# Performance work log

Hardware: AMD Instinct MI355X
Metric: run time of the kernel (lower is better)

The kernel has to match this reference:

```python
import jax, jax.numpy as jnp
import numpy as np


def deform_conv2d(x, w, offset, mask, pad):
    """Modulated deformable conv (DCNv2), stride 1, dilation 1, groups 1.
    x: [B,C,H,W], w: [Co,C,kh,kw], offset: [B,2*K,H,W] (y,x per tap), mask: [B,K,H,W].
    Output spatial size equals input (pad = (k-1)//2).
    """
    B, C, H, W = x.shape
    Co, _, kh, kw = w.shape
    K = kh * kw
    off = offset.reshape(B, K, 2, H, W)
    dy, dx = off[:, :, 0], off[:, :, 1]               # [B,K,H,W]
    ky, kx = jnp.meshgrid(jnp.arange(kh), jnp.arange(kw), indexing='ij')
    ky = ky.reshape(K).astype(x.dtype)
    kx = kx.reshape(K).astype(x.dtype)
    hh = jnp.arange(H, dtype=x.dtype)
    ww = jnp.arange(W, dtype=x.dtype)
    # sampling coords: p0 + p_k + delta p_k
    py = hh[None, None, :, None] - pad + ky[None, :, None, None] + dy  # [B,K,H,W]
    px = ww[None, None, None, :] - pad + kx[None, :, None, None] + dx
    y0 = jnp.floor(py)
    x0 = jnp.floor(px)
    wy = py - y0
    wx = px - x0
    y0i = y0.astype(jnp.int32)
    x0i = x0.astype(jnp.int32)
    x_flat = x.reshape(B, C, H * W)

    def gather(yi, xi):
        valid = (yi >= 0) & (yi < H) & (xi >= 0) & (xi < W)  # zero padding outside
        idx = jnp.clip(yi, 0, H - 1) * W + jnp.clip(xi, 0, W - 1)
        g = jnp.take_along_axis(x_flat, idx.reshape(B, 1, K * H * W), axis=2)
        g = g.reshape(B, C, K, H, W)
        return g * valid[:, None].astype(x.dtype)

    v00 = gather(y0i, x0i)
    v01 = gather(y0i, x0i + 1)
    v10 = gather(y0i + 1, x0i)
    v11 = gather(y0i + 1, x0i + 1)
    wy_ = wy[:, None]  # [B,1,K,H,W]
    wx_ = wx[:, None]
    samp = (v00 * (1 - wy_) * (1 - wx_) + v01 * (1 - wy_) * wx_
            + v10 * wy_ * (1 - wx_) + v11 * wy_ * wx_)   # [B,C,K,H,W]
    # masked weighted accumulation == conv over sampled taps
    return jnp.einsum('bckhw,bkhw,ock->bohw', samp, mask, w.reshape(Co, C, K))


def setup_inputs() -> dict:
    key = jax.random.key(0)
    ks = jax.random.split(key, 10)
    B, C, H, W, Co = 4, 64, 64, 64, 64
    inp = {
        'x': jax.random.normal(ks[0], (B, C, H, W), dtype=jnp.float32),
        'filter1': jax.random.normal(ks[1], (Co, C, 3, 3), dtype=jnp.float32) * 0.05,
        'offset1': jax.random.normal(ks[2], (B, 2 * 9, H, W), dtype=jnp.float32),
        'mask1': jax.random.uniform(ks[3], (B, 9, H, W), dtype=jnp.float32),
        'filter2': jax.random.normal(ks[4], (Co, C, 5, 5), dtype=jnp.float32) * 0.03,
        'offset2': jax.random.normal(ks[5], (B, 2 * 25, H, W), dtype=jnp.float32),
        'mask2': jax.random.uniform(ks[6], (B, 25, H, W), dtype=jnp.float32),
        'filter3': jax.random.normal(ks[7], (Co, C, 7, 7), dtype=jnp.float32) * 0.02,
        'offset3': jax.random.normal(ks[8], (B, 2 * 49, H, W), dtype=jnp.float32),
        'mask3': jax.random.uniform(ks[9], (B, 49, H, W), dtype=jnp.float32),
    }
    return inp


def reference(x, filter1, offset1, mask1, filter2, offset2, mask2, filter3, offset3, mask3):
    part1 = deform_conv2d(x, filter1, offset1, mask1, pad=1)  # 3x3
    part2 = deform_conv2d(x, filter2, offset2, mask2, pad=2)  # 5x5
    part3 = deform_conv2d(x, filter3, offset3, mask3, pad=3)  # 7x7
    return jnp.concatenate((part1, part2, part3), axis=1)
```

## Files before the change

kernel.cpp:

```cpp
#include <hip/hip_runtime.h>
#include <hip/hip_bf16.h>


typedef __attribute__((ext_vector_type(8))) short bf16x8;
typedef __attribute__((ext_vector_type(8))) unsigned short u16x8;
typedef __attribute__((ext_vector_type(4))) float f32x4;

#define WR 16
#define WC 30
#define WS 68
#define SLS 20

__device__ __forceinline__ float b2f(unsigned short u) {
    return __uint_as_float(((unsigned)u) << 16);
}
__device__ __forceinline__ unsigned short f2bf(float f) {
    __hip_bfloat16 h = __float2bfloat16(f);
    return *reinterpret_cast<unsigned short*>(&h);
}

__global__ __launch_bounds__(256) void k_prep(
    const float* __restrict__ x,
    const float* __restrict__ f1, const float* __restrict__ f2, const float* __restrict__ f3,
    unsigned short* __restrict__ xTb,
    unsigned short* __restrict__ wp1, unsigned short* __restrict__ wp2, unsigned short* __restrict__ wp3) {
    __shared__ float tile[64][65];
    int bid = blockIdx.x;
    int tid = threadIdx.x;
    if (bid < 256) {
        int b = bid >> 6, h = bid & 63;
        {
            int w = tid & 63, c4 = tid >> 6;
            const float* xp = x + (((b * 64) * 64 + h) * 64) + w;
            #pragma unroll
            for (int i = 0; i < 16; ++i) {
                int c = c4 * 16 + i;
                tile[c][w] = xp[c * 4096];
            }
        }
        __syncthreads();
        {
            int c = tid & 63, w4 = tid >> 6;
            unsigned short* op = xTb + (((b * 64 + h) * 64) * 64) + c;
            #pragma unroll
            for (int i = 0; i < 16; ++i) {
                int ww = w4 * 16 + i;
                op[ww * 64] = f2bf(tile[c][ww]);
            }
        }
    } else {
        int idx = (bid - 256) * 256 + tid;
        const float* f; unsigned short* wp; int K, rel;
        if (idx < 36864)       { f = f1; wp = wp1; K = 9;  rel = idx; }
        else if (idx < 139264) { f = f2; wp = wp2; K = 25; rel = idx - 36864; }
        else                   { f = f3; wp = wp3; K = 49; rel = idx - 139264; }
        int c = rel & 63;
        int o = (rel >> 6) & 63;
        int k = rel >> 12;
        wp[rel] = f2bf(f[(o * 64 + c) * K + k]);
    }
}

template<int KW, int PAD, int KS, int KE>
__device__ __forceinline__ void run_range(
    const float* __restrict__ offp, const float* __restrict__ mskp,
    const unsigned short* __restrict__ wp, const unsigned short* __restrict__ win,
    const unsigned short* __restrict__ xb,
    int h, int pw, int ylo, int cxlo, int ch0, int l16, f32x4 acc[4]) {

    #pragma unroll 2
    for (int k = KS; k < KE; ++k) {
        int ky = k / KW, kx = k - ky * KW;
        float dy = offp[k * 8192];
        float dx = offp[k * 8192 + 4096];
        float mk = mskp[k * 4096];
        float py = (float)(h - PAD + ky) + dy;
        float px = (float)(pw - PAD + kx) + dx;
        float y0f = floorf(py), x0f = floorf(px);
        float wy = py - y0f, wx = px - x0f;
        int y0 = (int)y0f, x0 = (int)x0f;
        int y1 = y0 + 1, x1 = x0 + 1;
        float fy0 = ((unsigned)y0 < 64u) ? (1.f - wy) * mk : 0.f;
        float fy1 = ((unsigned)y1 < 64u) ? wy * mk         : 0.f;
        float gx0 = ((unsigned)x0 < 64u) ? (1.f - wx)      : 0.f;
        float gx1 = ((unsigned)x1 < 64u) ? wx              : 0.f;
        float w00 = fy0 * gx0, w01 = fy0 * gx1, w10 = fy1 * gx0, w11 = fy1 * gx1;

        int r0 = y0 - ylo, r1 = r0 + 1;
        int c0 = x0 - cxlo, c1 = c0 + 1;
        bool oow = ((w00 != 0.f) & (((unsigned)r0 >= WR) | ((unsigned)c0 >= WC)))
                 | ((w01 != 0.f) & (((unsigned)r0 >= WR) | ((unsigned)c1 >= WC)))
                 | ((w10 != 0.f) & (((unsigned)r1 >= WR) | ((unsigned)c0 >= WC)))
                 | ((w11 != 0.f) & (((unsigned)r1 >= WR) | ((unsigned)c1 >= WC)));
        int r0c = min(max(r0, 0), WR - 1), r1c = min(max(r1, 0), WR - 1);
        int c0c = min(max(c0, 0), WC - 1), c1c = min(max(c1, 0), WC - 1);
        int p00 = (r0c * WC + c0c) * WS;
        int p01 = (r0c * WC + c1c) * WS;
        int p10 = (r1c * WC + c0c) * WS;
        int p11 = (r1c * WC + c1c) * WS;

        u16x8 g00a = *(const u16x8*)(win + p00 + ch0);
        u16x8 g01a = *(const u16x8*)(win + p01 + ch0);
        u16x8 g10a = *(const u16x8*)(win + p10 + ch0);
        u16x8 g11a = *(const u16x8*)(win + p11 + ch0);
        u16x8 g00b = *(const u16x8*)(win + p00 + 32 + ch0);
        u16x8 g01b = *(const u16x8*)(win + p01 + 32 + ch0);
        u16x8 g10b = *(const u16x8*)(win + p10 + 32 + ch0);
        u16x8 g11b = *(const u16x8*)(win + p11 + 32 + ch0);

        if (oow) {
            int y0g = min(max(y0, 0), 63), y1g = min(max(y1, 0), 63);
            int x0g = min(max(x0, 0), 63), x1g = min(max(x1, 0), 63);
            int o00 = ((y0g << 6) + x0g) << 6;
            int o01 = ((y0g << 6) + x1g) << 6;
            int o10 = ((y1g << 6) + x0g) << 6;
            int o11 = ((y1g << 6) + x1g) << 6;
            g00a = *(const u16x8*)(xb + o00 + ch0);
            g01a = *(const u16x8*)(xb + o01 + ch0);
            g10a = *(const u16x8*)(xb + o10 + ch0);
            g11a = *(const u16x8*)(xb + o11 + ch0);
            g00b = *(const u16x8*)(xb + o00 + 32 + ch0);
            g01b = *(const u16x8*)(xb + o01 + 32 + ch0);
            g10b = *(const u16x8*)(xb + o10 + 32 + ch0);
            g11b = *(const u16x8*)(xb + o11 + 32 + ch0);
        }

        union { bf16x8 v; unsigned short u[8]; } A0, A1;
        #pragma unroll
        for (int j = 0; j < 8; ++j) {
            float s0 = w00 * b2f(g00a[j]) + w01 * b2f(g01a[j])
                     + w10 * b2f(g10a[j]) + w11 * b2f(g11a[j]);
            float s1 = w00 * b2f(g00b[j]) + w01 * b2f(g01b[j])
                     + w10 * b2f(g10b[j]) + w11 * b2f(g11b[j]);
            A0.u[j] = f2bf(s0);
            A1.u[j] = f2bf(s1);
        }

        const unsigned short* wpk = wp + (k << 12);
        #pragma unroll
        for (int ct = 0; ct < 4; ++ct) {
            const unsigned short* wr = wpk + ((ct * 16 + l16) << 6);
            bf16x8 b0 = *(const bf16x8*)(wr + ch0);
            bf16x8 b1 = *(const bf16x8*)(wr + 32 + ch0);
            acc[ct] = __builtin_amdgcn_mfma_f32_16x16x32_bf16(A0.v, b0, acc[ct], 0, 0, 0);
            acc[ct] = __builtin_amdgcn_mfma_f32_16x16x32_bf16(A1.v, b1, acc[ct], 0, 0, 0);
        }
    }
}

__global__ __launch_bounds__(256) void k_dcn(
    const unsigned short* __restrict__ xTb,
    const float* __restrict__ off1, const float* __restrict__ msk1, const unsigned short* __restrict__ wp1,
    const float* __restrict__ off2, const float* __restrict__ msk2, const unsigned short* __restrict__ wp2,
    const float* __restrict__ off3, const float* __restrict__ msk3, const unsigned short* __restrict__ wp3,
    float* __restrict__ out) {

    __shared__ __align__(16) unsigned char smem[WR * WC * WS * 2];
    unsigned short* win = (unsigned short*)smem;
    float* slab = (float*)smem;

    int tile = blockIdx.x;
    int b  = tile >> 8;
    int h  = (tile >> 2) & 63;
    int w0 = (tile & 3) << 4;

    int tid  = threadIdx.x;
    int wv   = tid >> 6;
    int lane = tid & 63;
    int quad = lane >> 4;
    int l16  = lane & 15;
    int ylo  = h - 7, cxlo = w0 - 7;

    const unsigned short* xb = xTb + ((size_t)b << 18);

    {
        int j = tid & 7;
        for (int p = tid >> 3; p < WR * WC; p += 32) {
            int r = p / WC, cc = p - r * WC;
            int y = min(max(ylo + r, 0), 63);
            int x = min(max(cxlo + cc, 0), 63);
            *(u16x8*)(win + p * WS + j * 8) =
                *(const u16x8*)(xb + (((y << 6) + x) << 6) + j * 8);
        }
    }
    __syncthreads();

    int pw  = w0 + l16;
    int ch0 = quad << 3;
    const float* o1p = off1 + (b * 18) * 4096 + (h << 6) + pw;
    const float* m1p = msk1 + (b * 9)  * 4096 + (h << 6) + pw;
    const float* o2p = off2 + (b * 50) * 4096 + (h << 6) + pw;
    const float* m2p = msk2 + (b * 25) * 4096 + (h << 6) + pw;
    const float* o3p = off3 + (b * 98) * 4096 + (h << 6) + pw;
    const float* m3p = msk3 + (b * 49) * 4096 + (h << 6) + pw;

    f32x4 accA[4], accB[4];
    #pragma unroll
    for (int i = 0; i < 4; ++i) { accA[i] = (f32x4){0,0,0,0}; accB[i] = (f32x4){0,0,0,0}; }
    int slabA, slabB = -1;

    if (wv == 0) {
        run_range<3,1,0,9>  (o1p, m1p, wp1, win, xb, h, pw, ylo, cxlo, ch0, l16, accA);
        run_range<5,2,0,12> (o2p, m2p, wp2, win, xb, h, pw, ylo, cxlo, ch0, l16, accB);
        slabA = 0; slabB = 1;
    } else if (wv == 1) {
        run_range<5,2,12,25>(o2p, m2p, wp2, win, xb, h, pw, ylo, cxlo, ch0, l16, accA);
        run_range<7,3,0,8>  (o3p, m3p, wp3, win, xb, h, pw, ylo, cxlo, ch0, l16, accB);
        slabA = 2; slabB = 3;
    } else if (wv == 2) {
        run_range<7,3,8,29> (o3p, m3p, wp3, win, xb, h, pw, ylo, cxlo, ch0, l16, accA);
        slabA = 4;
    } else {
        run_range<7,3,29,49>(o3p, m3p, wp3, win, xb, h, pw, ylo, cxlo, ch0, l16, accA);
        slabA = 5;
    }

    __syncthreads();

    #pragma unroll
    for (int ct = 0; ct < 4; ++ct) {
        *(f32x4*)&slab[slabA * 1280 + (ct * 16 + l16) * SLS + quad * 4] = accA[ct];
    }
    if (slabB >= 0) {
        #pragma unroll
        for (int ct = 0; ct < 4; ++ct) {
            *(f32x4*)&slab[slabB * 1280 + (ct * 16 + l16) * SLS + quad * 4] = accB[ct];
        }
    }
    __syncthreads();

    for (int it = tid; it < 768; it += 256) {
        int g = it & 3;
        int o = it >> 2;
        int oo = o & 63;
        int base = oo * SLS + g * 4;
        f32x4 v;
        if (o < 64) {
            v = *(const f32x4*)&slab[base];
        } else if (o < 128) {
            f32x4 a0 = *(const f32x4*)&slab[1280 + base];
            f32x4 a1 = *(const f32x4*)&slab[2560 + base];
            #pragma unroll
            for (int r = 0; r < 4; ++r) v[r] = a0[r] + a1[r];
        } else {
            f32x4 a0 = *(const f32x4*)&slab[3840 + base];
            f32x4 a1 = *(const f32x4*)&slab[5120 + base];
            f32x4 a2 = *(const f32x4*)&slab[6400 + base];
            #pragma unroll
            for (int r = 0; r < 4; ++r) v[r] = a0[r] + (a1[r] + a2[r]);
        }
        *(f32x4*)&out[(((size_t)b * 192 + o) * 64 + h) * 64 + w0 + g * 4] = v;
    }
}

extern "C" void kernel_launch(void* const* d_in, const int* in_sizes, int n_in,
                              void* d_out, int out_size, void* d_ws, size_t ws_size,
                              hipStream_t stream) {
    const float* x    = (const float*)d_in[0];
    const float* f1   = (const float*)d_in[1];
    const float* off1 = (const float*)d_in[2];
    const float* msk1 = (const float*)d_in[3];
    const float* f2   = (const float*)d_in[4];
    const float* off2 = (const float*)d_in[5];
    const float* msk2 = (const float*)d_in[6];
    const float* f3   = (const float*)d_in[7];
    const float* off3 = (const float*)d_in[8];
    const float* msk3 = (const float*)d_in[9];
    float* out = (float*)d_out;

    unsigned short* xTb = (unsigned short*)d_ws;
    unsigned short* wp1 = xTb + 4 * 64 * 64 * 64;
    unsigned short* wp2 = wp1 + 9 * 4096;
    unsigned short* wp3 = wp2 + 25 * 4096;

    k_prep<<<dim3(1584), dim3(256), 0, stream>>>(x, f1, f2, f3, xTb, wp1, wp2, wp3);
    k_dcn<<<dim3(1024), dim3(256), 0, stream>>>(xTb,
                                                off1, msk1, wp1,
                                                off2, msk2, wp2,
                                                off3, msk3, wp3,
                                                out);
}
```

Before: 195.6 us.

## Split deformable taps across eight waves and pack bilinear math into float2

```diff
diff --git a/kernel.cpp b/kernel.cpp
--- a/kernel.cpp
+++ b/kernel.cpp
@@ -5,18 +5,22 @@
 typedef __attribute__((ext_vector_type(8))) short bf16x8;
 typedef __attribute__((ext_vector_type(8))) unsigned short u16x8;
 typedef __attribute__((ext_vector_type(4))) float f32x4;
+typedef __attribute__((ext_vector_type(2))) float f32x2;
 
 #define WR 16
 #define WC 30
 #define WS 68
 #define SLS 20
 
-__device__ __forceinline__ float b2f(unsigned short u) {
-    return __uint_as_float(((unsigned)u) << 16);
-}
 __device__ __forceinline__ unsigned short f2bf(float f) {
     __hip_bfloat16 h = __float2bfloat16(f);
     return *reinterpret_cast<unsigned short*>(&h);
+}
+__device__ __forceinline__ f32x2 unpk(unsigned u) {
+    f32x2 r;
+    r[0] = __uint_as_float(u << 16);
+    r[1] = __uint_as_float(u & 0xffff0000u);
+    return r;
 }
 
 __global__ __launch_bounds__(256) void k_prep(
@@ -99,14 +103,16 @@
         int p10 = (r1c * WC + c0c) * WS;
         int p11 = (r1c * WC + c1c) * WS;
 
-        u16x8 g00a = *(const u16x8*)(win + p00 + ch0);
-        u16x8 g01a = *(const u16x8*)(win + p01 + ch0);
-        u16x8 g10a = *(const u16x8*)(win + p10 + ch0);
-        u16x8 g11a = *(const u16x8*)(win + p11 + ch0);
-        u16x8 g00b = *(const u16x8*)(win + p00 + 32 + ch0);
-        u16x8 g01b = *(const u16x8*)(win + p01 + 32 + ch0);
-        u16x8 g10b = *(const u16x8*)(win + p10 + 32 + ch0);
-        u16x8 g11b = *(const u16x8*)(win + p11 + 32 + ch0);
+        union U { u16x8 v; unsigned u[4]; };
+        U g00a, g01a, g10a, g11a, g00b, g01b, g10b, g11b;
+        g00a.v = *(const u16x8*)(win + p00 + ch0);
+        g01a.v = *(const u16x8*)(win + p01 + ch0);
+        g10a.v = *(const u16x8*)(win + p10 + ch0);
+        g11a.v = *(const u16x8*)(win + p11 + ch0);
+        g00b.v = *(const u16x8*)(win + p00 + 32 + ch0);
+        g01b.v = *(const u16x8*)(win + p01 + 32 + ch0);
+        g10b.v = *(const u16x8*)(win + p10 + 32 + ch0);
+        g11b.v = *(const u16x8*)(win + p11 + 32 + ch0);
 
         if (oow) {
             int y0g = min(max(y0, 0), 63), y1g = min(max(y1, 0), 63);
@@ -115,25 +121,28 @@
             int o01 = ((y0g << 6) + x1g) << 6;
             int o10 = ((y1g << 6) + x0g) << 6;
             int o11 = ((y1g << 6) + x1g) << 6;
-            g00a = *(const u16x8*)(xb + o00 + ch0);
-            g01a = *(const u16x8*)(xb + o01 + ch0);
-            g10a = *(const u16x8*)(xb + o10 + ch0);
-            g11a = *(const u16x8*)(xb + o11 + ch0);
-            g00b = *(const u16x8*)(xb + o00 + 32 + ch0);
-            g01b = *(const u16x8*)(xb + o01 + 32 + ch0);
-            g10b = *(const u16x8*)(xb + o10 + 32 + ch0);
-            g11b = *(const u16x8*)(xb + o11 + 32 + ch0);
-        }
-
+            g00a.v = *(const u16x8*)(xb + o00 + ch0);
+            g01a.v = *(const u16x8*)(xb + o01 + ch0);
+            g10a.v = *(const u16x8*)(xb + o10 + ch0);
+            g11a.v = *(const u16x8*)(xb + o11 + ch0);
+            g00b.v = *(const u16x8*)(xb + o00 + 32 + ch0);
+            g01b.v = *(const u16x8*)(xb + o01 + 32 + ch0);
+            g10b.v = *(const u16x8*)(xb + o10 + 32 + ch0);
+            g11b.v = *(const u16x8*)(xb + o11 + 32 + ch0);
+        }
+
+        f32x2 W00 = {w00, w00}, W01 = {w01, w01}, W10 = {w10, w10}, W11 = {w11, w11};
         union { bf16x8 v; unsigned short u[8]; } A0, A1;
         #pragma unroll
-        for (int j = 0; j < 8; ++j) {
-            float s0 = w00 * b2f(g00a[j]) + w01 * b2f(g01a[j])
-                     + w10 * b2f(g10a[j]) + w11 * b2f(g11a[j]);
-            float s1 = w00 * b2f(g00b[j]) + w01 * b2f(g01b[j])
-                     + w10 * b2f(g10b[j]) + w11 * b2f(g11b[j]);
-            A0.u[j] = f2bf(s0);
-            A1.u[j] = f2bf(s1);
+        for (int j2 = 0; j2 < 4; ++j2) {
+            f32x2 s0 = W00 * unpk(g00a.u[j2]) + W01 * unpk(g01a.u[j2])
+                     + W10 * unpk(g10a.u[j2]) + W11 * unpk(g11a.u[j2]);
+            f32x2 s1 = W00 * unpk(g00b.u[j2]) + W01 * unpk(g01b.u[j2])
+                     + W10 * unpk(g10b.u[j2]) + W11 * unpk(g11b.u[j2]);
+            A0.u[2 * j2]     = f2bf(s0[0]);
+            A0.u[2 * j2 + 1] = f2bf(s0[1]);
+            A1.u[2 * j2]     = f2bf(s1[0]);
+            A1.u[2 * j2 + 1] = f2bf(s1[1]);
         }
 
         const unsigned short* wpk = wp + (k << 12);
@@ -148,7 +157,7 @@
     }
 }
 
-__global__ __launch_bounds__(256) void k_dcn(
+__global__ __launch_bounds__(512, 4) void k_dcn(
     const unsigned short* __restrict__ xTb,
     const float* __restrict__ off1, const float* __restrict__ msk1, const unsigned short* __restrict__ wp1,
     const float* __restrict__ off2, const float* __restrict__ msk2, const unsigned short* __restrict__ wp2,
@@ -175,7 +184,7 @@
 
     {
         int j = tid & 7;
-        for (int p = tid >> 3; p < WR * WC; p += 32) {
+        for (int p = tid >> 3; p < WR * WC; p += 64) {
             int r = p / WC, cc = p - r * WC;
             int y = min(max(ylo + r, 0), 63);
             int x = min(max(cxlo + cc, 0), 63);
@@ -199,20 +208,33 @@
     for (int i = 0; i < 4; ++i) { accA[i] = (f32x4){0,0,0,0}; accB[i] = (f32x4){0,0,0,0}; }
     int slabA, slabB = -1;
 
-    if (wv == 0) {
-        run_range<3,1,0,9>  (o1p, m1p, wp1, win, xb, h, pw, ylo, cxlo, ch0, l16, accA);
-        run_range<5,2,0,12> (o2p, m2p, wp2, win, xb, h, pw, ylo, cxlo, ch0, l16, accB);
-        slabA = 0; slabB = 1;
-    } else if (wv == 1) {
-        run_range<5,2,12,25>(o2p, m2p, wp2, win, xb, h, pw, ylo, cxlo, ch0, l16, accA);
-        run_range<7,3,0,8>  (o3p, m3p, wp3, win, xb, h, pw, ylo, cxlo, ch0, l16, accB);
-        slabA = 2; slabB = 3;
-    } else if (wv == 2) {
-        run_range<7,3,8,29> (o3p, m3p, wp3, win, xb, h, pw, ylo, cxlo, ch0, l16, accA);
-        slabA = 4;
-    } else {
-        run_range<7,3,29,49>(o3p, m3p, wp3, win, xb, h, pw, ylo, cxlo, ch0, l16, accA);
-        slabA = 5;
+    switch (wv) {
+        case 0:
+            run_range<3,1,0,9>  (o1p, m1p, wp1, win, xb, h, pw, ylo, cxlo, ch0, l16, accA);
+            slabA = 0; break;
+        case 1:
+            run_range<5,2,0,11> (o2p, m2p, wp2, win, xb, h, pw, ylo, cxlo, ch0, l16, accA);
+            slabA = 1; break;
+        case 2:
+            run_range<5,2,11,22>(o2p, m2p, wp2, win, xb, h, pw, ylo, cxlo, ch0, l16, accA);
+            slabA = 2; break;
+        case 3:
+            run_range<5,2,22,25>(o2p, m2p, wp2, win, xb, h, pw, ylo, cxlo, ch0, l16, accA);
+            slabA = 3;
+            run_range<7,3,0,8>  (o3p, m3p, wp3, win, xb, h, pw, ylo, cxlo, ch0, l16, accB);
+            slabB = 4; break;
+        case 4:
+            run_range<7,3,8,18> (o3p, m3p, wp3, win, xb, h, pw, ylo, cxlo, ch0, l16, accA);
+            slabA = 5; break;
+        case 5:
+            run_range<7,3,18,28>(o3p, m3p, wp3, win, xb, h, pw, ylo, cxlo, ch0, l16, accA);
+            slabA = 6; break;
+        case 6:
+            run_range<7,3,28,38>(o3p, m3p, wp3, win, xb, h, pw, ylo, cxlo, ch0, l16, accA);
+            slabA = 7; break;
+        default:
+            run_range<7,3,38,49>(o3p, m3p, wp3, win, xb, h, pw, ylo, cxlo, ch0, l16, accA);
+            slabA = 8; break;
     }
 
     __syncthreads();
@@ -229,7 +251,7 @@
     }
     __syncthreads();
 
-    for (int it = tid; it < 768; it += 256) {
+    for (int it = tid; it < 768; it += 512) {
         int g = it & 3;
         int o = it >> 2;
         int oo = o & 63;
@@ -238,16 +260,19 @@
         if (o < 64) {
             v = *(const f32x4*)&slab[base];
         } else if (o < 128) {
-            f32x4 a0 = *(const f32x4*)&slab[1280 + base];
-            f32x4 a1 = *(const f32x4*)&slab[2560 + base];
-            #pragma unroll
-            for (int r = 0; r < 4; ++r) v[r] = a0[r] + a1[r];
-        } else {
-            f32x4 a0 = *(const f32x4*)&slab[3840 + base];
-            f32x4 a1 = *(const f32x4*)&slab[5120 + base];
-            f32x4 a2 = *(const f32x4*)&slab[6400 + base];
+            f32x4 a0 = *(const f32x4*)&slab[1 * 1280 + base];
+            f32x4 a1 = *(const f32x4*)&slab[2 * 1280 + base];
+            f32x4 a2 = *(const f32x4*)&slab[3 * 1280 + base];
             #pragma unroll
             for (int r = 0; r < 4; ++r) v[r] = a0[r] + (a1[r] + a2[r]);
+        } else {
+            f32x4 a0 = *(const f32x4*)&slab[4 * 1280 + base];
+            f32x4 a1 = *(const f32x4*)&slab[5 * 1280 + base];
+            f32x4 a2 = *(const f32x4*)&slab[6 * 1280 + base];
+            f32x4 a3 = *(const f32x4*)&slab[7 * 1280 + base];
+            f32x4 a4 = *(const f32x4*)&slab[8 * 1280 + base];
+            #pragma unroll
+            for (int r = 0; r < 4; ++r) v[r] = (a0[r] + a1[r]) + (a2[r] + a3[r]) + a4[r];
         }
         *(f32x4*)&out[(((size_t)b * 192 + o) * 64 + h) * 64 + w0 + g * 4] = v;
     }
@@ -274,7 +299,7 @@
     unsigned short* wp3 = wp2 + 25 * 4096;
 
     k_prep<<<dim3(1584), dim3(256), 0, stream>>>(x, f1, f2, f3, xTb, wp1, wp2, wp3);
-    k_dcn<<<dim3(1024), dim3(256), 0, stream>>>(xTb,
+    k_dcn<<<dim3(1024), dim3(512), 0, stream>>>(xTb,
                                                 off1, msk1, wp1,
                                                 off2, msk2, wp2,
                                                 off3, msk3, wp3,
```

Measured after the change: 180.3 us. -7.9%, faster.

## Split channel halves and tap ranges across 16 waves per block

Applied to the files above, without the earlier changes.

```diff
diff --git a/kernel.cpp b/kernel.cpp
--- a/kernel.cpp
+++ b/kernel.cpp
@@ -5,18 +5,22 @@
 typedef __attribute__((ext_vector_type(8))) short bf16x8;
 typedef __attribute__((ext_vector_type(8))) unsigned short u16x8;
 typedef __attribute__((ext_vector_type(4))) float f32x4;
+typedef __attribute__((ext_vector_type(2))) float f32x2;
 
 #define WR 16
 #define WC 30
 #define WS 68
 #define SLS 20
 
-__device__ __forceinline__ float b2f(unsigned short u) {
-    return __uint_as_float(((unsigned)u) << 16);
-}
 __device__ __forceinline__ unsigned short f2bf(float f) {
     __hip_bfloat16 h = __float2bfloat16(f);
     return *reinterpret_cast<unsigned short*>(&h);
+}
+__device__ __forceinline__ f32x2 unpk(unsigned u) {
+    f32x2 r;
+    r[0] = __uint_as_float(u << 16);
+    r[1] = __uint_as_float(u & 0xffff0000u);
+    return r;
 }
 
 __global__ __launch_bounds__(256) void k_prep(
@@ -68,9 +72,9 @@
     const unsigned short* __restrict__ xb,
     int h, int pw, int ylo, int cxlo, int ch0, int l16, f32x4 acc[4]) {
 
-    #pragma unroll 2
+    #pragma unroll
     for (int k = KS; k < KE; ++k) {
-        int ky = k / KW, kx = k - ky * KW;
+        const int ky = k / KW, kx = k - ky * KW;
         float dy = offp[k * 8192];
         float dx = offp[k * 8192 + 4096];
         float mk = mskp[k * 4096];
@@ -94,61 +98,42 @@
                  | ((w11 != 0.f) & (((unsigned)r1 >= WR) | ((unsigned)c1 >= WC)));
         int r0c = min(max(r0, 0), WR - 1), r1c = min(max(r1, 0), WR - 1);
         int c0c = min(max(c0, 0), WC - 1), c1c = min(max(c1, 0), WC - 1);
-        int p00 = (r0c * WC + c0c) * WS;
-        int p01 = (r0c * WC + c1c) * WS;
-        int p10 = (r1c * WC + c0c) * WS;
-        int p11 = (r1c * WC + c1c) * WS;
-
-        u16x8 g00a = *(const u16x8*)(win + p00 + ch0);
-        u16x8 g01a = *(const u16x8*)(win + p01 + ch0);
-        u16x8 g10a = *(const u16x8*)(win + p10 + ch0);
-        u16x8 g11a = *(const u16x8*)(win + p11 + ch0);
-        u16x8 g00b = *(const u16x8*)(win + p00 + 32 + ch0);
-        u16x8 g01b = *(const u16x8*)(win + p01 + 32 + ch0);
-        u16x8 g10b = *(const u16x8*)(win + p10 + 32 + ch0);
-        u16x8 g11b = *(const u16x8*)(win + p11 + 32 + ch0);
+
+        union GU { u16x8 v; unsigned u[4]; } g00, g01, g10, g11;
+        g00.v = *(const u16x8*)(win + (r0c * WC + c0c) * WS + ch0);
+        g01.v = *(const u16x8*)(win + (r0c * WC + c1c) * WS + ch0);
+        g10.v = *(const u16x8*)(win + (r1c * WC + c0c) * WS + ch0);
+        g11.v = *(const u16x8*)(win + (r1c * WC + c1c) * WS + ch0);
 
         if (oow) {
             int y0g = min(max(y0, 0), 63), y1g = min(max(y1, 0), 63);
             int x0g = min(max(x0, 0), 63), x1g = min(max(x1, 0), 63);
-            int o00 = ((y0g << 6) + x0g) << 6;
-            int o01 = ((y0g << 6) + x1g) << 6;
-            int o10 = ((y1g << 6) + x0g) << 6;
-            int o11 = ((y1g << 6) + x1g) << 6;
-            g00a = *(const u16x8*)(xb + o00 + ch0);
-            g01a = *(const u16x8*)(xb + o01 + ch0);
-            g10a = *(const u16x8*)(xb + o10 + ch0);
-            g11a = *(const u16x8*)(xb + o11 + ch0);
-            g00b = *(const u16x8*)(xb + o00 + 32 + ch0);
-            g01b = *(const u16x8*)(xb + o01 + 32 + ch0);
-            g10b = *(const u16x8*)(xb + o10 + 32 + ch0);
-            g11b = *(const u16x8*)(xb + o11 + 32 + ch0);
-        }
-
-        union { bf16x8 v; unsigned short u[8]; } A0, A1;
-        #pragma unroll
-        for (int j = 0; j < 8; ++j) {
-            float s0 = w00 * b2f(g00a[j]) + w01 * b2f(g01a[j])
-                     + w10 * b2f(g10a[j]) + w11 * b2f(g11a[j]);
-            float s1 = w00 * b2f(g00b[j]) + w01 * b2f(g01b[j])
-                     + w10 * b2f(g10b[j]) + w11 * b2f(g11b[j]);
-            A0.u[j] = f2bf(s0);
-            A1.u[j] = f2bf(s1);
+            g00.v = *(const u16x8*)(xb + (((y0g << 6) + x0g) << 6) + ch0);
+            g01.v = *(const u16x8*)(xb + (((y0g << 6) + x1g) << 6) + ch0);
+            g10.v = *(const u16x8*)(xb + (((y1g << 6) + x0g) << 6) + ch0);
+            g11.v = *(const u16x8*)(xb + (((y1g << 6) + x1g) << 6) + ch0);
+        }
+
+        f32x2 W00 = {w00, w00}, W01 = {w01, w01}, W10 = {w10, w10}, W11 = {w11, w11};
+        union { bf16x8 v; unsigned short u[8]; } A;
+        #pragma unroll
+        for (int j = 0; j < 4; ++j) {
+            f32x2 s = W00 * unpk(g00.u[j]) + W01 * unpk(g01.u[j])
+                    + W10 * unpk(g10.u[j]) + W11 * unpk(g11.u[j]);
+            A.u[2 * j]     = f2bf(s[0]);
+            A.u[2 * j + 1] = f2bf(s[1]);
         }
 
         const unsigned short* wpk = wp + (k << 12);
         #pragma unroll
         for (int ct = 0; ct < 4; ++ct) {
-            const unsigned short* wr = wpk + ((ct * 16 + l16) << 6);
-            bf16x8 b0 = *(const bf16x8*)(wr + ch0);
-            bf16x8 b1 = *(const bf16x8*)(wr + 32 + ch0);
-            acc[ct] = __builtin_amdgcn_mfma_f32_16x16x32_bf16(A0.v, b0, acc[ct], 0, 0, 0);
-            acc[ct] = __builtin_amdgcn_mfma_f32_16x16x32_bf16(A1.v, b1, acc[ct], 0, 0, 0);
-        }
-    }
-}
-
-__global__ __launch_bounds__(256) void k_dcn(
+            bf16x8 bfr = *(const bf16x8*)(wpk + ((ct * 16 + l16) << 6) + ch0);
+            acc[ct] = __builtin_amdgcn_mfma_f32_16x16x32_bf16(A.v, bfr, acc[ct], 0, 0, 0);
+        }
+    }
+}
+
+__global__ __launch_bounds__(1024, 8) void k_dcn(
     const unsigned short* __restrict__ xTb,
     const float* __restrict__ off1, const float* __restrict__ msk1, const unsigned short* __restrict__ wp1,
     const float* __restrict__ off2, const float* __restrict__ msk2, const unsigned short* __restrict__ wp2,
@@ -164,18 +149,20 @@
     int h  = (tile >> 2) & 63;
     int w0 = (tile & 3) << 4;
 
-    int tid  = threadIdx.x;
-    int wv   = tid >> 6;
-    int lane = tid & 63;
-    int quad = lane >> 4;
-    int l16  = lane & 15;
-    int ylo  = h - 7, cxlo = w0 - 7;
+    int tid   = threadIdx.x;
+    int wv    = tid >> 6;
+    int chunk = wv >> 1;
+    int half  = wv & 1;
+    int lane  = tid & 63;
+    int quad  = lane >> 4;
+    int l16   = lane & 15;
+    int ylo   = h - 7, cxlo = w0 - 7;
 
     const unsigned short* xb = xTb + ((size_t)b << 18);
 
     {
         int j = tid & 7;
-        for (int p = tid >> 3; p < WR * WC; p += 32) {
+        for (int p = tid >> 3; p < WR * WC; p += 128) {
             int r = p / WC, cc = p - r * WC;
             int y = min(max(ylo + r, 0), 63);
             int x = min(max(cxlo + cc, 0), 63);
@@ -186,7 +173,7 @@
     __syncthreads();
 
     int pw  = w0 + l16;
-    int ch0 = quad << 3;
+    int ch0 = half * 32 + (quad << 3);
     const float* o1p = off1 + (b * 18) * 4096 + (h << 6) + pw;
     const float* m1p = msk1 + (b * 9)  * 4096 + (h << 6) + pw;
     const float* o2p = off2 + (b * 50) * 4096 + (h << 6) + pw;
@@ -194,60 +181,63 @@
     const float* o3p = off3 + (b * 98) * 4096 + (h << 6) + pw;
     const float* m3p = msk3 + (b * 49) * 4096 + (h << 6) + pw;
 
-    f32x4 accA[4], accB[4];
+    f32x4 acc[4];
     #pragma unroll
-    for (int i = 0; i < 4; ++i) { accA[i] = (f32x4){0,0,0,0}; accB[i] = (f32x4){0,0,0,0}; }
-    int slabA, slabB = -1;
-
-    if (wv == 0) {
-        run_range<3,1,0,9>  (o1p, m1p, wp1, win, xb, h, pw, ylo, cxlo, ch0, l16, accA);
-        run_range<5,2,0,12> (o2p, m2p, wp2, win, xb, h, pw, ylo, cxlo, ch0, l16, accB);
-        slabA = 0; slabB = 1;
-    } else if (wv == 1) {
-        run_range<5,2,12,25>(o2p, m2p, wp2, win, xb, h, pw, ylo, cxlo, ch0, l16, accA);
-        run_range<7,3,0,8>  (o3p, m3p, wp3, win, xb, h, pw, ylo, cxlo, ch0, l16, accB);
-        slabA = 2; slabB = 3;
-    } else if (wv == 2) {
-        run_range<7,3,8,29> (o3p, m3p, wp3, win, xb, h, pw, ylo, cxlo, ch0, l16, accA);
-        slabA = 4;
-    } else {
-        run_range<7,3,29,49>(o3p, m3p, wp3, win, xb, h, pw, ylo, cxlo, ch0, l16, accA);
-        slabA = 5;
-    }
-
-    __syncthreads();
-
-    #pragma unroll
-    for (int ct = 0; ct < 4; ++ct) {
-        *(f32x4*)&slab[slabA * 1280 + (ct * 16 + l16) * SLS + quad * 4] = accA[ct];
-    }
-    if (slabB >= 0) {
+    for (int i = 0; i < 4; ++i) acc[i] = (f32x4){0.f, 0.f, 0.f, 0.f};
+
+    switch (chunk) {
+        case 0:  run_range<3,1,0,9>  (o1p, m1p, wp1, win, xb, h, pw, ylo, cxlo, ch0, l16, acc); break;
+        case 1:  run_range<5,2,0,12> (o2p, m2p, wp2, win, xb, h, pw, ylo, cxlo, ch0, l16, acc); break;
+        case 2:  run_range<5,2,12,25>(o2p, m2p, wp2, win, xb, h, pw, ylo, cxlo, ch0, l16, acc); break;
+        case 3:  run_range<7,3,0,10> (o3p, m3p, wp3, win, xb, h, pw, ylo, cxlo, ch0, l16, acc); break;
+        case 4:  run_range<7,3,10,20>(o3p, m3p, wp3, win, xb, h, pw, ylo, cxlo, ch0, l16, acc); break;
+        case 5:  run_range<7,3,20,30>(o3p, m3p, wp3, win, xb, h, pw, ylo, cxlo, ch0, l16, acc); break;
+        case 6:  run_range<7,3,30,40>(o3p, m3p, wp3, win, xb, h, pw, ylo, cxlo, ch0, l16, acc); break;
+        default: run_range<7,3,40,49>(o3p, m3p, wp3, win, xb, h, pw, ylo, cxlo, ch0, l16, acc); break;
+    }
+
+    __syncthreads();
+
+    if (half == 0) {
         #pragma unroll
         for (int ct = 0; ct < 4; ++ct) {
-            *(f32x4*)&slab[slabB * 1280 + (ct * 16 + l16) * SLS + quad * 4] = accB[ct];
-        }
-    }
-    __syncthreads();
-
-    for (int it = tid; it < 768; it += 256) {
-        int g = it & 3;
-        int o = it >> 2;
+            *(f32x4*)&slab[chunk * 1280 + (ct * 16 + l16) * SLS + quad * 4] = acc[ct];
+        }
+    }
+    __syncthreads();
+    if (half == 1) {
+        #pragma unroll
+        for (int ct = 0; ct < 4; ++ct) {
+            float* p = &slab[chunk * 1280 + (ct * 16 + l16) * SLS + quad * 4];
+            f32x4 old = *(f32x4*)p;
+            #pragma unroll
+            for (int r = 0; r < 4; ++r) old[r] += acc[ct][r];
+            *(f32x4*)p = old;
+        }
+    }
+    __syncthreads();
+
+    if (tid < 768) {
+        int g = tid & 3;
+        int o = tid >> 2;
         int oo = o & 63;
         int base = oo * SLS + g * 4;
         f32x4 v;
         if (o < 64) {
             v = *(const f32x4*)&slab[base];
         } else if (o < 128) {
-            f32x4 a0 = *(const f32x4*)&slab[1280 + base];
-            f32x4 a1 = *(const f32x4*)&slab[2560 + base];
+            f32x4 a0 = *(const f32x4*)&slab[1 * 1280 + base];
+            f32x4 a1 = *(const f32x4*)&slab[2 * 1280 + base];
             #pragma unroll
             for (int r = 0; r < 4; ++r) v[r] = a0[r] + a1[r];
         } else {
-            f32x4 a0 = *(const f32x4*)&slab[3840 + base];
-            f32x4 a1 = *(const f32x4*)&slab[5120 + base];
-            f32x4 a2 = *(const f32x4*)&slab[6400 + base];
-            #pragma unroll
-            for (int r = 0; r < 4; ++r) v[r] = a0[r] + (a1[r] + a2[r]);
+            f32x4 a0 = *(const f32x4*)&slab[3 * 1280 + base];
+            f32x4 a1 = *(const f32x4*)&slab[4 * 1280 + base];
+            f32x4 a2 = *(const f32x4*)&slab[5 * 1280 + base];
+            f32x4 a3 = *(const f32x4*)&slab[6 * 1280 + base];
+            f32x4 a4 = *(const f32x4*)&slab[7 * 1280 + base];
+            #pragma unroll
+            for (int r = 0; r < 4; ++r) v[r] = (a0[r] + a1[r]) + (a2[r] + a3[r]) + a4[r];
         }
         *(f32x4*)&out[(((size_t)b * 192 + o) * 64 + h) * 64 + w0 + g * 4] = v;
     }
@@ -274,9 +264,9 @@
     unsigned short* wp3 = wp2 + 25 * 4096;
 
     k_prep<<<dim3(1584), dim3(256), 0, stream>>>(x, f1, f2, f3, xTb, wp1, wp2, wp3);
-    k_dcn<<<dim3(1024), dim3(256), 0, stream>>>(xTb,
-                                                off1, msk1, wp1,
-                                                off2, msk2, wp2,
-                                                off3, msk3, wp3,
-                                                out);
-}
+    k_dcn<<<dim3(1024), dim3(1024), 0, stream>>>(xTb,
+                                                 off1, msk1, wp1,
+                                                 off2, msk2, wp2,
+                                                 off3, msk3, wp3,
+                                                 out);
+}
```

Result: no change. 196.5 us (+0.4%).
